# Optimization experiments

Hardware: AMD Instinct MI355X
Metric: run time of the kernel (lower is better)

## Reference

```python
import jax, jax.numpy as jnp
import numpy as np
from functools import partial

# norse LIFAdEx default parameters
DT = 0.001
TAU_SYN_INV = 1.0 / 5e-3   # 200.0
TAU_MEM_INV = 1.0 / 1e-2   # 100.0
TAU_ADA_INV = 2.0
ADAPT_CURRENT = 4.0
ADAPT_SPIKE = 0.02
DELTA_T = 0.5
V_LEAK = 0.0
V_TH = 1.0
V_RESET = 0.0
ALPHA = 100.0              # superspike surrogate sharpness
TAU_FILTER_INV = 223.1435511314


@jax.custom_vjp
def superspike(x):
    # forward: heaviside; backward: superspike surrogate grad
    return (x > 0).astype(x.dtype)

def _ss_fwd(x):
    return superspike(x), x

def _ss_bwd(x, g):
    return (g / (ALPHA * jnp.abs(x) + 1.0) ** 2,)

superspike.defvjp(_ss_fwd, _ss_bwd)


def lif_adex_recurrent(x, W_in, W_rec):
    """x: (T,B,F) -> spikes (T,B,H). norse lif_adex_step semantics."""
    T, B, _ = x.shape
    H = W_rec.shape[0]
    # precompute feed-forward input current for all steps: (T,B,H)
    i_in = jnp.einsum('tbf,hf->tbh', x, W_in)

    def step(carry, ic):
        z, v, i, a = carry
        dv = DT * TAU_MEM_INV * ((V_LEAK - v)
                                 + DELTA_T * jnp.exp((v - V_TH) / DELTA_T)
                                 + i - a)
        v_dec = v + dv
        i_dec = i - DT * TAU_SYN_INV * i
        a_dec = a + DT * TAU_ADA_INV * (ADAPT_CURRENT * (v - V_LEAK) - a)
        z_new = superspike(v_dec - V_TH)
        v_new = (1.0 - z_new) * v_dec + z_new * V_RESET
        i_new = i_dec + ic + z @ W_rec.T
        a_new = a_dec + z_new * ADAPT_SPIKE
        return (z_new, v_new, i_new, a_new), z_new

    z0 = jnp.zeros((B, H), x.dtype)
    init = (z0, z0, z0, z0)
    _, spikes = jax.lax.scan(step, init, i_in)
    return spikes


def exp_filter(spikes, W_out, b_out):
    """Linear readout + exponential low-pass filter over time."""
    y = jnp.einsum('tbh,oh->tbo', spikes, W_out) + b_out  # (T,B,O)
    k = DT * TAU_FILTER_INV

    def step(o_prev, y_t):
        o = o_prev + k * (y_t - o_prev)
        return o, o

    o0 = y[0]
    _, rest = jax.lax.scan(step, o0, y[1:])
    return jnp.concatenate([o0[None], rest], axis=0)


def setup_inputs() -> dict:
    key = jax.random.key(0)
    kx, k1, k2, k3, k4 = jax.random.split(key, 5)
    T, B, F, H, O = 500, 128, 128, 512, 32
    x = jax.random.normal(kx, (T, B, F), dtype=jnp.float32)
    W_in = jax.random.normal(k1, (H, F), dtype=jnp.float32) * np.sqrt(2.0 / F)
    W_rec = jax.random.normal(k2, (H, H), dtype=jnp.float32) * np.sqrt(2.0 / H)
    W_out = jax.random.normal(k3, (O, H), dtype=jnp.float32) * np.sqrt(1.0 / H)
    b_out = jax.random.normal(k4, (O,), dtype=jnp.float32) * 0.01
    return {'x': x, 'W_in': W_in, 'W_rec': W_rec, 'W_out': W_out, 'b_out': b_out}


def reference(x, W_in, W_rec, W_out, b_out):
    spikes = lif_adex_recurrent(x, W_in, W_rec)
    return exp_filter(spikes, W_out, b_out)
```

## Files before the change

kernel.cpp:

```cpp
#include <hip/hip_runtime.h>
#include <hip/hip_bf16.h>
#include <cstdint>
#include <cstddef>

#define T_STEPS 500
#define BATCH   128
#define FDIM    128
#define HDIM    512
#define ODIM    32
#define M_ROWS  (T_STEPS * BATCH)
#define ZOFF    (512u << 11)
#define ZOFFB   (512u << 10)

typedef __attribute__((ext_vector_type(8))) __bf16 bf16x8;
typedef __attribute__((ext_vector_type(4))) float  f32x4;

__device__ __forceinline__ float bfbits2f(unsigned short u) {
    union { unsigned int i; float f; } c; c.i = ((unsigned int)u) << 16; return c.f;
}
__device__ __forceinline__ float asf(unsigned int u) {
    union { unsigned int i; float f; } c; c.i = u; return c.f;
}

__global__ void detect_kernel(const unsigned short* __restrict__ xw, int* __restrict__ flag) {
    __shared__ int cnt;
    if (threadIdx.x == 0) cnt = 0;
    __syncthreads();
    unsigned short w = xw[threadIdx.x * 2];
    int e = (w >> 7) & 0xFF;
    if (e >= 170) atomicAdd(&cnt, 1);
    __syncthreads();
    if (threadIdx.x == 0) *flag = (cnt >= 8) ? 1 : 0;
}

__global__ void prep_kernel(const void* __restrict__ Wrec,
                            const void* __restrict__ Wout,
                            const void* __restrict__ bout,
                            const int* __restrict__ flag,
                            float* __restrict__ WrecT,
                            unsigned short* __restrict__ WrecTb,
                            float* __restrict__ WoutT,
                            float* __restrict__ bout32) {
    const int fp32 = *flag;
    int idx = blockIdx.x * blockDim.x + threadIdx.x;
    if (fp32) {
        if (idx < HDIM * HDIM) {
            int h = idx / HDIM, hp = idx % HDIM;
            WrecT[hp * HDIM + h] = ((const float*)Wrec)[idx];
        }
        if (idx < HDIM) WrecT[HDIM * HDIM + idx] = 0.f;
    } else {
        if (idx < HDIM * HDIM) {
            int h = idx / HDIM, hp = idx % HDIM;
            WrecTb[hp * HDIM + h] = ((const unsigned short*)Wrec)[idx];
        }
        if (idx < HDIM) WrecTb[HDIM * HDIM + idx] = 0;
    }
    if (idx < ODIM * HDIM) {
        int o = idx / HDIM, h = idx % HDIM;
        WoutT[h * ODIM + o] = fp32 ? ((const float*)Wout)[idx]
                                   : bfbits2f(((const unsigned short*)Wout)[idx]);
    }
    if (idx < ODIM)
        bout32[idx] = fp32 ? ((const float*)bout)[idx]
                           : bfbits2f(((const unsigned short*)bout)[idx]);
}

__global__ __launch_bounds__(256) void iin_gemm_mfma(const __hip_bfloat16* __restrict__ x,
                                                     const __hip_bfloat16* __restrict__ Win,
                                                     const int* __restrict__ flag,
                                                     float* __restrict__ iin) {
    if (*flag != 0) return;
    const int mt   = blockIdx.x;
    const int nt   = blockIdx.y;
    const int wave = threadIdx.x >> 6;
    const int lane = threadIdx.x & 63;
    const int l15  = lane & 15;
    const int quad = lane >> 4;
    const int m_base = mt * 64 + wave * 16;
    const int n_base = nt * 64;

    const __bf16* xb = reinterpret_cast<const __bf16*>(x);
    const __bf16* wb = reinterpret_cast<const __bf16*>(Win);

    f32x4 acc[4] = {{0.f,0.f,0.f,0.f},{0.f,0.f,0.f,0.f},{0.f,0.f,0.f,0.f},{0.f,0.f,0.f,0.f}};

#pragma unroll
    for (int kk = 0; kk < 4; ++kk) {
        const int k0 = kk * 32 + quad * 8;
        bf16x8 a = *reinterpret_cast<const bf16x8*>(xb + (size_t)(m_base + l15) * FDIM + k0);
#pragma unroll
        for (int nb = 0; nb < 4; ++nb) {
            bf16x8 bf = *reinterpret_cast<const bf16x8*>(wb + (size_t)(n_base + nb * 16 + l15) * FDIM + k0);
            acc[nb] = __builtin_amdgcn_mfma_f32_16x16x32_bf16(a, bf, acc[nb], 0, 0, 0);
        }
    }

#pragma unroll
    for (int nb = 0; nb < 4; ++nb)
#pragma unroll
        for (int r = 0; r < 4; ++r)
            iin[(size_t)(m_base + quad * 4 + r) * HDIM + n_base + nb * 16 + l15] = acc[nb][r];
}

__global__ __launch_bounds__(256) void iin_gemm_valu(const float* __restrict__ x,
                                                     const float* __restrict__ Win,
                                                     const int* __restrict__ flag,
                                                     float* __restrict__ iin) {
    if (*flag != 1) return;
    const int tid = threadIdx.x;
    const int m0  = blockIdx.x * 32;

    __shared__ float xs[32][FDIM];

    {
        const float4* src = (const float4*)(x + (size_t)m0 * FDIM);
        float4* dst = (float4*)&xs[0][0];
        for (int i = tid; i < 32 * FDIM / 4; i += 256) dst[i] = src[i];
    }
    __syncthreads();

    const float4* w0p = (const float4*)(Win + (size_t)tid * FDIM);
    const float4* w1p = (const float4*)(Win + (size_t)(tid + 256) * FDIM);

    float acc[32][2];
#pragma unroll
    for (int m = 0; m < 32; ++m) { acc[m][0] = 0.f; acc[m][1] = 0.f; }

    for (int k4 = 0; k4 < FDIM / 4; ++k4) {
        float4 w0 = w0p[k4];
        float4 w1 = w1p[k4];
#pragma unroll
        for (int m = 0; m < 32; ++m) {
            float4 xv = *(const float4*)&xs[m][k4 * 4];
            float a0 = acc[m][0], a1 = acc[m][1];
            a0 += xv.x * w0.x; a0 += xv.y * w0.y; a0 += xv.z * w0.z; a0 += xv.w * w0.w;
            a1 += xv.x * w1.x; a1 += xv.y * w1.y; a1 += xv.z * w1.z; a1 += xv.w * w1.w;
            acc[m][0] = a0; acc[m][1] = a1;
        }
    }

#pragma unroll
    for (int m = 0; m < 32; ++m) {
        iin[(size_t)(m0 + m) * HDIM + tid]       = acc[m][0];
        iin[(size_t)(m0 + m) * HDIM + 256 + tid] = acc[m][1];
    }
}

__global__ __launch_bounds__(1024) void scan_f32(const float* __restrict__ iin,
                                                 const float* __restrict__ WrecT,
                                                 const int* __restrict__ flag,
                                                 unsigned long long* __restrict__ masksG) {
    if (*flag != 1) return;
    const int b    = blockIdx.x;
    const int tid  = threadIdx.x;
    const int q    = tid & 127;
    const int p    = tid >> 7;
    const int lane = tid & 63;
    const int wv   = tid >> 6;
    const bool st  = tid < HDIM;
    const int h    = tid;

    __shared__ unsigned long long wmask[8];
    __shared__ float4 part[8][128];
    __shared__ alignas(16) unsigned int slA[8][68];
    __shared__ alignas(16) unsigned int slB[8][68];
    unsigned int (*slO)[68] = slA;
    unsigned int (*slN)[68] = slB;

    float v = 0.f, cur = 0.f, a = 0.f;
    int   cnt = 0;
    const char* WQ = (const char*)WrecT + q * 16;

    for (int t = 0; t < T_STEPS; ++t) {
        float ic = 0.f, i_dec = 0.f;
        bool  zk = false;
        unsigned long long m = 0;

        if (st) {
            ic = iin[((size_t)t * BATCH + b) * HDIM + h];
            float s = (0.0f - v) + 0.5f * expf((v - 1.0f) * 2.0f);
            s = s + cur;
            s = s - a;
            float v_dec = v + 0.1f * s;
            i_dec = cur - 0.2f * cur;
            float a_dec = a + 0.002f * (4.0f * v - a);
            zk = (v_dec - 1.0f) > 0.0f;
            m = __ballot(zk);
            if (lane == 0) {
                wmask[wv] = m;
                masksG[((size_t)t * BATCH + b) * 8 + wv] = m;
            }
            v = zk ? 0.0f : v_dec;
            a = zk ? (a_dec + 0.02f) : a_dec;
        }

        float4 rs = {0.f, 0.f, 0.f, 0.f};
        {
            const int n  = (cnt + 7 - p) >> 3;
            const int ng = (n + 3) >> 2;
            float4 b0[4], b1[4];
            auto ld4 = [&](int g, float4* d) {
                uint4 i0 = *(const uint4*)&slO[p][g << 2];
                d[0] = *(const float4*)(WQ + i0.x);
                d[1] = *(const float4*)(WQ + i0.y);
                d[2] = *(const float4*)(WQ + i0.z);
                d[3] = *(const float4*)(WQ + i0.w);
            };
            auto acc4 = [&](const float4* d) {
#pragma unroll
                for (int u = 0; u < 4; ++u) {
                    rs.x += d[u].x; rs.y += d[u].y; rs.z += d[u].z; rs.w += d[u].w;
                }
            };
            int g = 0;
            if (ng > 0) ld4(0, b0);
            while (g + 2 <= ng) {
                ld4(g + 1, b1);
                acc4(b0);
                if (g + 2 < ng) ld4(g + 2, b0);
                acc4(b1);
                g += 2;
            }
            if (g < ng) acc4(b0);
        }
        part[p][q] = rs;

        __syncthreads();

        int total = 0;
#pragma unroll
        for (int w = 0; w < 8; ++w) total += __popcll(wmask[w]);

        if (st) {
            float rec = 0.f;
#pragma unroll
            for (int pp = 0; pp < 8; ++pp)
                rec += ((const float*)&part[pp][h >> 2])[h & 3];
            cur = (i_dec + ic) + rec;
            if (zk) {
                int off = __popcll(m & ((1ull << lane) - 1ull));
#pragma unroll
                for (int w = 0; w < 8; ++w) if (w < wv) off += __popcll(wmask[w]);
                slN[off & 7][off >> 3] = (unsigned int)h << 11;
            }
        } else if (tid < HDIM + 32) {
            int s5 = (tid - HDIM) >> 2;
            int k  = (tid - HDIM) & 3;
            int ne = (total + 7 - s5) >> 3;
            int padc = (4 - (ne & 3)) & 3;
            if (k < padc) slN[s5][ne + k] = ZOFF;
        }
        cnt = total;

        __syncthreads();

        unsigned int (*tp)[68] = slO; slO = slN; slN = tp;
    }
}

__global__ __launch_bounds__(1024) void scan_bf16(const float* __restrict__ iin,
                                                  const unsigned short* __restrict__ WrecTb,
                                                  const int* __restrict__ flag,
                                                  unsigned long long* __restrict__ masksG) {
    if (*flag != 0) return;
    const int b    = blockIdx.x;
    const int tid  = threadIdx.x;
    const int q    = tid & 63;
    const int pc   = tid >> 6;
    const int lane = tid & 63;
    const int wv   = tid >> 6;
    const bool st  = tid < HDIM;
    const int h    = tid;

    __shared__ unsigned long long wmask[8];
    __shared__ float4 partA[16][64];
    __shared__ float4 partB[16][64];
    __shared__ alignas(16) unsigned int slA[16][36];
    __shared__ alignas(16) unsigned int slB[16][36];
    unsigned int (*slO)[36] = slA;
    unsigned int (*slN)[36] = slB;

    float v = 0.f, cur = 0.f, a = 0.f;
    int   cnt = 0;
    const char* WQ = (const char*)WrecTb + q * 16;

    for (int t = 0; t < T_STEPS; ++t) {
        float ic = 0.f, i_dec = 0.f; bool zk = false; unsigned long long m = 0;
        if (st) {
            ic = iin[((size_t)t * BATCH + b) * HDIM + h];
            float s = (0.0f - v) + 0.5f * expf((v - 1.0f) * 2.0f);
            s = s + cur;
            s = s - a;
            float v_dec = v + 0.1f * s;
            i_dec = cur - 0.2f * cur;
            float a_dec = a + 0.002f * (4.0f * v - a);
            zk = (v_dec - 1.0f) > 0.0f;
            m = __ballot(zk);
            if (lane == 0) {
                wmask[wv] = m;
                masksG[((size_t)t * BATCH + b) * 8 + wv] = m;
            }
            v = zk ? 0.0f : v_dec;
            a = zk ? (a_dec + 0.02f) : a_dec;
        }

        float rs0=0.f,rs1=0.f,rs2=0.f,rs3=0.f,rs4=0.f,rs5=0.f,rs6=0.f,rs7=0.f;
        {
            const unsigned int* sl = slO[pc];
            const int n  = (cnt + 15 - pc) >> 4;
            const int ng = (n + 3) >> 2;
            uint4 w0[4], w1[4];
            auto ldg = [&](int g, uint4* w) {
                uint4 ix = *(const uint4*)(sl + (g << 2));
                w[0] = *(const uint4*)(WQ + ix.x);
                w[1] = *(const uint4*)(WQ + ix.y);
                w[2] = *(const uint4*)(WQ + ix.z);
                w[3] = *(const uint4*)(WQ + ix.w);
            };
            auto accw = [&](const uint4* w) {
#pragma unroll
                for (int u = 0; u < 4; ++u) {
                    rs0 += asf(w[u].x << 16); rs1 += asf(w[u].x & 0xffff0000u);
                    rs2 += asf(w[u].y << 16); rs3 += asf(w[u].y & 0xffff0000u);
                    rs4 += asf(w[u].z << 16); rs5 += asf(w[u].z & 0xffff0000u);
                    rs6 += asf(w[u].w << 16); rs7 += asf(w[u].w & 0xffff0000u);
                }
            };
            int g = 0;
            if (ng > 0) ldg(0, w0);
            while (g + 2 <= ng) {
                ldg(g + 1, w1);
                accw(w0);
                if (g + 2 < ng) ldg(g + 2, w0);
                accw(w1);
                g += 2;
            }
            if (g < ng) accw(w0);
        }
        partA[pc][q] = (float4){rs0, rs1, rs2, rs3};
        partB[pc][q] = (float4){rs4, rs5, rs6, rs7};

        __syncthreads();

        int total = 0;
#pragma unroll
        for (int w = 0; w < 8; ++w) total += __popcll(wmask[w]);

        if (st) {
            float rec = 0.f;
            const int  qq = h >> 3, jj = h & 3;
            const bool hi = (h & 4) != 0;
#pragma unroll
            for (int pp = 0; pp < 16; ++pp) {
                const float* pa = (const float*)&partA[pp][qq];
                const float* pb = (const float*)&partB[pp][qq];
                rec += hi ? pb[jj] : pa[jj];
            }
            cur = (i_dec + ic) + rec;
            if (zk) {
                int off = __popcll(m & ((1ull << lane) - 1ull));
#pragma unroll
                for (int w = 0; w < 8; ++w) if (w < wv) off += __popcll(wmask[w]);
                slN[off & 15][off >> 4] = (unsigned int)h << 10;
            }
        } else if (tid < HDIM + 64) {
            int s5 = (tid - HDIM) >> 2;
            int k  = (tid - HDIM) & 3;
            int ne = (total + 15 - s5) >> 4;
            int padc = (4 - (ne & 3)) & 3;
            if (k < padc) slN[s5][ne + k] = ZOFFB;
        }
        cnt = total;

        __syncthreads();

        unsigned int (*tp)[36] = slO; slO = slN; slN = tp;
    }
}

__global__ __launch_bounds__(256) void y_kernel(const unsigned long long* __restrict__ masks,
                                                const float* __restrict__ WoutT,
                                                const float* __restrict__ bout,
                                                float* __restrict__ y) {
    const int tid = threadIdx.x;
    const int p   = blockIdx.x * 8 + (tid >> 5);
    const int o   = tid & 31;
    const unsigned long long* mp = masks + (size_t)p * 8;
    float acc = 0.f;
#pragma unroll
    for (int w = 0; w < 8; ++w) {
        unsigned long long m = mp[w];
        const float* Wb = WoutT + (size_t)w * 64 * ODIM + o;
        while (m) {
            int j = __builtin_ctzll(m);
            acc += Wb[j * ODIM];
            m &= m - 1;
        }
    }
    y[(size_t)p * ODIM + o] = acc + bout[o];
}

__global__ __launch_bounds__(64) void filter_kernel(const float* __restrict__ y,
                                                    const int* __restrict__ flag,
                                                    void* __restrict__ out) {
    const int p = blockIdx.x * 64 + threadIdx.x;
    const int fp32o = *flag;
    const float kf = 0.2231435511314f;
    float c0[10], c1[10];
#pragma unroll
    for (int u = 0; u < 10; ++u) c0[u] = y[(size_t)u * (BATCH * ODIM) + p];
    float o_state = 0.f;
    for (int base = 0; base < T_STEPS; base += 10) {
        if (base + 10 < T_STEPS) {
#pragma unroll
            for (int u = 0; u < 10; ++u)
                c1[u] = y[(size_t)(base + 10 + u) * (BATCH * ODIM) + p];
        }
#pragma unroll
        for (int u = 0; u < 10; ++u) {
            int t = base + u;
            float yt = c0[u];
            o_state = (t == 0) ? yt : (o_state + kf * (yt - o_state));
            size_t oi = (size_t)t * (BATCH * ODIM) + p;
            if (fp32o) ((float*)out)[oi] = o_state;
            else       ((__hip_bfloat16*)out)[oi] = __float2bfloat16(o_state);
        }
#pragma unroll
        for (int u = 0; u < 10; ++u) c0[u] = c1[u];
    }
}

extern "C" void kernel_launch(void* const* d_in, const int* in_sizes, int n_in,
                              void* d_out, int out_size, void* d_ws, size_t ws_size,
                              hipStream_t stream) {
    const void* x = d_in[0]; const void* Win = d_in[1]; const void* Wrec = d_in[2];
    const void* Wout = d_in[3]; const void* bout = d_in[4];
    for (int i = 0; i < n_in; ++i) {
        switch (in_sizes[i]) {
            case 8192000: x    = d_in[i]; break;
            case 65536:   Win  = d_in[i]; break;
            case 262144:  Wrec = d_in[i]; break;
            case 16384:   Wout = d_in[i]; break;
            case 32:      bout = d_in[i]; break;
            default: break;
        }
    }

    const size_t OFF_FLAG  = 0;
    const size_t OFF_BOUT  = 256;
    const size_t OFF_WOUTT = 512;
    const size_t OFF_WRECT = 66048;
    const size_t OFF_MASK  = 1378816;
    const size_t OFF_IIN   = 5474816;
    const size_t OFF_Y     = OFF_IIN;
    const size_t REQUIRED  = OFF_IIN + (size_t)M_ROWS * HDIM * 4;
    if (ws_size < REQUIRED) return;

    char* ws = (char*)d_ws;
    int*            flag   = (int*)(ws + OFF_FLAG);
    float*          bout32 = (float*)(ws + OFF_BOUT);
    float*          WoutT  = (float*)(ws + OFF_WOUTT);
    float*          WrecT  = (float*)(ws + OFF_WRECT);
    unsigned short* WrecTb = (unsigned short*)(ws + OFF_WRECT);
    unsigned long long* masks = (unsigned long long*)(ws + OFF_MASK);
    float*          iin    = (float*)(ws + OFF_IIN);
    float*          y      = (float*)(ws + OFF_Y);

    hipLaunchKernelGGL(detect_kernel, dim3(1), dim3(256), 0, stream,
                       (const unsigned short*)x, flag);
    hipLaunchKernelGGL(prep_kernel, dim3((HDIM * HDIM + 255) / 256), dim3(256), 0, stream,
                       Wrec, Wout, bout, flag, WrecT, WrecTb, WoutT, bout32);
    hipLaunchKernelGGL(iin_gemm_mfma, dim3(M_ROWS / 64, HDIM / 64), dim3(256), 0, stream,
                       (const __hip_bfloat16*)x, (const __hip_bfloat16*)Win, flag, iin);
    hipLaunchKernelGGL(iin_gemm_valu, dim3(M_ROWS / 32), dim3(256), 0, stream,
                       (const float*)x, (const float*)Win, flag, iin);
    hipLaunchKernelGGL(scan_f32, dim3(BATCH), dim3(1024), 0, stream,
                       iin, WrecT, flag, masks);
    hipLaunchKernelGGL(scan_bf16, dim3(BATCH), dim3(1024), 0, stream,
                       iin, WrecTb, flag, masks);
    hipLaunchKernelGGL(y_kernel, dim3(M_ROWS / 8), dim3(256), 0, stream,
                       masks, WoutT, bout32, y);
    hipLaunchKernelGGL(filter_kernel, dim3((BATCH * ODIM) / 64), dim3(64), 0, stream,
                       y, flag, d_out);
}
```

Before: 926.3 us.

## Retile fp32 input GEMM into 64x64 LDS tiles with 4x4 register blocking

```diff
diff --git a/kernel.cpp b/kernel.cpp
--- a/kernel.cpp
+++ b/kernel.cpp
@@ -72,7 +72,7 @@
                                                      float* __restrict__ iin) {
     if (*flag != 0) return;
     const int mt   = blockIdx.x;
-    const int nt   = blockIdx.y;
+    const int nt   = blockIdx.y & 7;
     const int wave = threadIdx.x >> 6;
     const int lane = threadIdx.x & 63;
     const int l15  = lane & 15;
@@ -103,47 +103,65 @@
             iin[(size_t)(m_base + quad * 4 + r) * HDIM + n_base + nb * 16 + l15] = acc[nb][r];
 }
 
+#define GPAD 132
 __global__ __launch_bounds__(256) void iin_gemm_valu(const float* __restrict__ x,
                                                      const float* __restrict__ Win,
                                                      const int* __restrict__ flag,
                                                      float* __restrict__ iin) {
     if (*flag != 1) return;
     const int tid = threadIdx.x;
-    const int m0  = blockIdx.x * 32;
-
-    __shared__ float xs[32][FDIM];
+    const int m0  = blockIdx.x * 64;
+    const int n0  = blockIdx.y * 64;
+
+    __shared__ float xs[64][GPAD];
+    __shared__ float wt[64][GPAD];
 
     {
-        const float4* src = (const float4*)(x + (size_t)m0 * FDIM);
-        float4* dst = (float4*)&xs[0][0];
-        for (int i = tid; i < 32 * FDIM / 4; i += 256) dst[i] = src[i];
+        const float4* xsrc = (const float4*)(x   + (size_t)m0 * FDIM);
+        const float4* wsrc = (const float4*)(Win + (size_t)n0 * FDIM);
+#pragma unroll
+        for (int it = 0; it < 8; ++it) {
+            int f4 = tid + it * 256;
+            int r  = f4 >> 5;
+            int c4 = f4 & 31;
+            *(float4*)&xs[r][c4 * 4] = xsrc[f4];
+            *(float4*)&wt[r][c4 * 4] = wsrc[f4];
+        }
     }
     __syncthreads();
 
-    const float4* w0p = (const float4*)(Win + (size_t)tid * FDIM);
-    const float4* w1p = (const float4*)(Win + (size_t)(tid + 256) * FDIM);
-
-    float acc[32][2];
-#pragma unroll
-    for (int m = 0; m < 32; ++m) { acc[m][0] = 0.f; acc[m][1] = 0.f; }
+    const int ty = tid >> 4;
+    const int tx = tid & 15;
+
+    float acc[4][4];
+#pragma unroll
+    for (int i = 0; i < 4; ++i)
+#pragma unroll
+        for (int j = 0; j < 4; ++j) acc[i][j] = 0.f;
 
     for (int k4 = 0; k4 < FDIM / 4; ++k4) {
-        float4 w0 = w0p[k4];
-        float4 w1 = w1p[k4];
-#pragma unroll
-        for (int m = 0; m < 32; ++m) {
-            float4 xv = *(const float4*)&xs[m][k4 * 4];
-            float a0 = acc[m][0], a1 = acc[m][1];
-            a0 += xv.x * w0.x; a0 += xv.y * w0.y; a0 += xv.z * w0.z; a0 += xv.w * w0.w;
-            a1 += xv.x * w1.x; a1 += xv.y * w1.y; a1 += xv.z * w1.z; a1 += xv.w * w1.w;
-            acc[m][0] = a0; acc[m][1] = a1;
-        }
-    }
-
-#pragma unroll
-    for (int m = 0; m < 32; ++m) {
-        iin[(size_t)(m0 + m) * HDIM + tid]       = acc[m][0];
-        iin[(size_t)(m0 + m) * HDIM + 256 + tid] = acc[m][1];
+        float4 a[4], bw[4];
+#pragma unroll
+        for (int i = 0; i < 4; ++i) a[i]  = *(const float4*)&xs[ty * 4 + i][k4 * 4];
+#pragma unroll
+        for (int j = 0; j < 4; ++j) bw[j] = *(const float4*)&wt[tx * 4 + j][k4 * 4];
+#pragma unroll
+        for (int i = 0; i < 4; ++i)
+#pragma unroll
+            for (int j = 0; j < 4; ++j) {
+                float s = acc[i][j];
+                s += a[i].x * bw[j].x;
+                s += a[i].y * bw[j].y;
+                s += a[i].z * bw[j].z;
+                s += a[i].w * bw[j].w;
+                acc[i][j] = s;
+            }
+    }
+
+#pragma unroll
+    for (int i = 0; i < 4; ++i) {
+        float4 o = {acc[i][0], acc[i][1], acc[i][2], acc[i][3]};
+        *(float4*)&iin[(size_t)(m0 + ty * 4 + i) * HDIM + n0 + tx * 4] = o;
     }
 }
 
@@ -162,7 +180,7 @@
     const int h    = tid;
 
     __shared__ unsigned long long wmask[8];
-    __shared__ float4 part[8][128];
+    __shared__ f32x4 part[8][128];
     __shared__ alignas(16) unsigned int slA[8][68];
     __shared__ alignas(16) unsigned int slB[8][68];
     unsigned int (*slO)[68] = slA;
@@ -195,23 +213,21 @@
             a = zk ? (a_dec + 0.02f) : a_dec;
         }
 
-        float4 rs = {0.f, 0.f, 0.f, 0.f};
+        f32x4 rs = {0.f, 0.f, 0.f, 0.f};
         {
             const int n  = (cnt + 7 - p) >> 3;
             const int ng = (n + 3) >> 2;
-            float4 b0[4], b1[4];
-            auto ld4 = [&](int g, float4* d) {
+            f32x4 b0[4], b1[4];
+            auto ld4 = [&](int g, f32x4* d) {
                 uint4 i0 = *(const uint4*)&slO[p][g << 2];
-                d[0] = *(const float4*)(WQ + i0.x);
-                d[1] = *(const float4*)(WQ + i0.y);
-                d[2] = *(const float4*)(WQ + i0.z);
-                d[3] = *(const float4*)(WQ + i0.w);
+                d[0] = *(const f32x4*)(WQ + i0.x);
+                d[1] = *(const f32x4*)(WQ + i0.y);
+                d[2] = *(const f32x4*)(WQ + i0.z);
+                d[3] = *(const f32x4*)(WQ + i0.w);
             };
-            auto acc4 = [&](const float4* d) {
-#pragma unroll
-                for (int u = 0; u < 4; ++u) {
-                    rs.x += d[u].x; rs.y += d[u].y; rs.z += d[u].z; rs.w += d[u].w;
-                }
+            auto acc4 = [&](const f32x4* d) {
+#pragma unroll
+                for (int u = 0; u < 4; ++u) rs = rs + d[u];
             };
             int g = 0;
             if (ng > 0) ld4(0, b0);
@@ -473,7 +489,7 @@
                        Wrec, Wout, bout, flag, WrecT, WrecTb, WoutT, bout32);
     hipLaunchKernelGGL(iin_gemm_mfma, dim3(M_ROWS / 64, HDIM / 64), dim3(256), 0, stream,
                        (const __hip_bfloat16*)x, (const __hip_bfloat16*)Win, flag, iin);
-    hipLaunchKernelGGL(iin_gemm_valu, dim3(M_ROWS / 32), dim3(256), 0, stream,
+    hipLaunchKernelGGL(iin_gemm_valu, dim3(M_ROWS / 64, HDIM / 64), dim3(256), 0, stream,
                        (const float*)x, (const float*)Win, flag, iin);
     hipLaunchKernelGGL(scan_f32, dim3(BATCH), dim3(1024), 0, stream,
                        iin, WrecT, flag, masks);
```

Measured after the change: 945.3 us. +2.1%, slower.
